# Performance work log

Hardware: AMD Instinct MI355X
Metric: run time of the kernel (lower is better)

The kernel has to match this reference:

```python
import jax, jax.numpy as jnp
import numpy as np

N = 6144
IN_F = 256
OUT_F = 64
ALPHA = 0.2  # leaky relu slope
NEG_INF = -9e15
ADJ_DENSITY = 0.01


def setup_inputs() -> dict:
    key = jax.random.key(0)
    kx, ka, kw, kat, ks, ke = jax.random.split(key, 6)
    x = jax.random.normal(kx, (N, IN_F), dtype=jnp.float32)
    adj = (jax.random.uniform(ka, (N, N)) < ADJ_DENSITY).astype(jnp.float32)
    adj = adj.at[jnp.arange(N), jnp.arange(N)].set(0.0)
    # xavier-uniform-ish init scale (gain 1.414)
    def xavier(k, shape):
        fan_in, fan_out = shape[0], shape[1]
        lim = 1.414 * np.sqrt(6.0 / (fan_in + fan_out))
        return jax.random.uniform(k, shape, minval=-lim, maxval=lim, dtype=jnp.float32)
    W = xavier(kw, (IN_F, OUT_F))
    a = xavier(kat, (2 * OUT_F, 1))
    W_si = xavier(ks, (1, 1))
    W_ei = xavier(ke, (1, 1))
    return {"x": x, "adj": adj, "W": W, "a": a, "W_si": W_si, "W_ei": W_ei}


def reference(x, adj, W, a, W_si, W_ei):
    # h: [N, F_out]
    h = x @ W
    # additive GAT score: e[i,j] = leakyrelu(Wh1[i] + Wh2[j])
    Wh1 = h @ a[:OUT_F, :]           # [N, 1]
    Wh2 = h @ a[OUT_F:, :]           # [N, 1]
    e = jax.nn.leaky_relu(Wh1 + Wh2.T, negative_slope=ALPHA)  # [N, N]
    # adjacency-power topology bias
    adj2 = adj @ adj
    adj3 = adj2 @ adj
    adj_w = adj + adj2 + adj3
    adj_w = adj_w.at[jnp.arange(N), jnp.arange(N)].set(0.0)
    e = jnp.abs(W_ei) * e + jnp.abs(W_si) * adj_w
    # masked softmax over neighbors (row-wise)
    scores = jnp.where(adj > 0, e, NEG_INF)
    attention = jax.nn.softmax(scores, axis=1)
    # dropout omitted (eval mode / training=False)
    h_prime = attention @ h
    return jax.nn.elu(h_prime)
```

## Files before the change

### kernel.cpp

```cpp
#include <hip/hip_runtime.h>
#include <math.h>

#define N 6144
#define MAXD 128
#define NWORDS 96
#define NW32 192

typedef unsigned long long u64;
typedef unsigned int u32;
typedef unsigned char u8;
typedef float f4 __attribute__((ext_vector_type(4)));


__device__ __forceinline__ int a_addr(int j) {
    int vdx = (j & ~255) | ((j & 3) << 6) | ((j >> 2) & 63);
    return (((vdx >> 2) & 7) << 10) | ((vdx >> 5) << 2) | (vdx & 3);
}

#define FA(s, c, a, b, ci) { u32 _t = (a) ^ (b); (s) = _t ^ (ci); (c) = ((a) & (b)) | ((ci) & _t); }

template <int START>
__device__ __forceinline__ void badd_from(u32* p, u32 cy) {
    #pragma unroll
    for (int q = START; q < 6; ++q) { u32 x = p[q] & cy; p[q] ^= cy; cy = x; }
    p[6] ^= cy;
}

__device__ __forceinline__ void csa15(u32* p, const u32* x) {
    u32 s0,c0,s1,c1,s2,c2,s3,c3,s4,c4;
    FA(s0,c0, x[0], x[1], x[2]);
    FA(s1,c1, x[3], x[4], x[5]);
    FA(s2,c2, x[6], x[7], x[8]);
    FA(s3,c3, x[9], x[10], x[11]);
    FA(s4,c4, x[12], x[13], x[14]);
    u32 t0,d0,u0,d1;
    FA(t0,d0, s0, s1, s2);
    FA(u0,d1, s3, s4, t0);
    u32 e0,f0,e1,f1,e2,f2;
    FA(e0,f0, c0, c1, c2);
    FA(e1,f1, c3, c4, d0);
    FA(e2,f2, e0, e1, d1);
    u32 g0,h0;
    FA(g0,h0, f0, f1, f2);
    badd_from<0>(p, u0);
    badd_from<1>(p, e2);
    badd_from<2>(p, g0);
    badd_from<3>(p, h0);
}

__device__ __forceinline__ u64 bit_transpose64(u64 x, int lane) {
    const u64 masks[6] = {0xAAAAAAAAAAAAAAAAull, 0xCCCCCCCCCCCCCCCCull,
                          0xF0F0F0F0F0F0F0F0ull, 0xFF00FF00FF00FF00ull,
                          0xFFFF0000FFFF0000ull, 0xFFFFFFFF00000000ull};
    #pragma unroll
    for (int k = 0; k < 6; ++k) {
        int s = 1 << k;
        u64 m = masks[k];
        u64 y = (u64)__shfl_xor((long long)x, s, 64);
        x = (lane & s) ? ((x & m) | ((y & m) >> s))
                       : ((x & ~m) | ((y & ~m) << s));
    }
    return x;
}

__global__ __launch_bounds__(256) void k_gemm_h(
    const float* __restrict__ x, const float* __restrict__ W,
    const float* __restrict__ a,
    float* __restrict__ h, float* __restrict__ Wh1, float* __restrict__ Wh2)
{
    __shared__ float Wl[256 * 64];
    int t = threadIdx.x;
    #pragma unroll
    for (int c = 0; c < 64; ++c) Wl[c * 256 + t] = W[c * 256 + t];
    __syncthreads();

    int w = t >> 6, lane = t & 63;
    int i0 = blockIdx.x * 32 + w * 8;
    const float* xr = x + (long)i0 * 256;

    float acc[8] = {0.f, 0.f, 0.f, 0.f, 0.f, 0.f, 0.f, 0.f};
    for (int k0 = 0; k0 < 256; k0 += 4) {
        float4 xv[8];
        #pragma unroll
        for (int r = 0; r < 8; ++r)
            xv[r] = *(const float4*)(xr + (long)r * 256 + k0);
        #pragma unroll
        for (int kk = 0; kk < 4; ++kk) {
            float wv = Wl[(k0 + kk) * 64 + lane];
            #pragma unroll
            for (int r = 0; r < 8; ++r) {
                float xs = (kk == 0) ? xv[r].x : (kk == 1) ? xv[r].y
                         : (kk == 2) ? xv[r].z : xv[r].w;
                acc[r] = fmaf(xs, wv, acc[r]);
            }
        }
    }

    #pragma unroll
    for (int r = 0; r < 8; ++r) {
        int i = i0 + r;
        h[(long)i * 64 + lane] = acc[r];
        float s1 = acc[r] * a[lane];
        float s2 = acc[r] * a[64 + lane];
        #pragma unroll
        for (int off = 32; off; off >>= 1) {
            s1 += __shfl_xor(s1, off, 64);
            s2 += __shfl_xor(s2, off, 64);
        }
        if (lane == 0) { Wh1[i] = s1; Wh2[i] = s2; }
    }
}

__global__ __launch_bounds__(256) void k_build(
    const float* __restrict__ adj,
    u64* __restrict__ rowbits, int* __restrict__ row_cnt, int* __restrict__ row_list)
{
    int i = blockIdx.x;
    int t = threadIdx.x, w = t >> 6, lane = t & 63;
    __shared__ int wtot[4];

    const f4* ar = (const f4*)(adj + (long)i * N) + (w * 6) * 64;

    f4 v[6];
    #pragma unroll
    for (int c = 0; c < 6; ++c)
        v[c] = __builtin_nontemporal_load(ar + c * 64 + lane);

    u64 m[6][4];
    #pragma unroll
    for (int c = 0; c < 6; ++c) {
        m[c][0] = __ballot(v[c].x != 0.0f);
        m[c][1] = __ballot(v[c].y != 0.0f);
        m[c][2] = __ballot(v[c].z != 0.0f);
        m[c][3] = __ballot(v[c].w != 0.0f);
    }

    int tot = 0;
    #pragma unroll
    for (int c = 0; c < 6; ++c) {
        #pragma unroll
        for (int p = 0; p < 4; ++p) tot += __popcll(m[c][p]);
    }
    if (lane == 0) wtot[w] = tot;
    __syncthreads();
    int base = 0;
    #pragma unroll
    for (int q = 0; q < 4; ++q) if (q < w) base += wtot[q];

    u64* rb = rowbits + (long)i * NWORDS + w * 24;
    #pragma unroll
    for (int c = 0; c < 6; ++c) {
        #pragma unroll
        for (int p = 0; p < 4; ++p) {
            u64 mm = m[c][p];
            if (lane == 0) rb[c * 4 + p] = mm;
            if ((mm >> lane) & 1ull) {
                int rank = __popcll(mm & ((1ull << lane) - 1ull));
                int s = base + rank;
                int j = (w * 6 + c) * 256 + (lane << 2) + p;
                if (s < MAXD) row_list[(long)i * MAXD + s] = j;
            }
            base += __popcll(mm);
        }
    }
    if (t == 0) {
        int tt = wtot[0] + wtot[1] + wtot[2] + wtot[3];
        row_cnt[i] = tt < 127 ? tt : 127;
    }
}

__global__ __launch_bounds__(256) void k_trans(
    const u64* __restrict__ rowbits, u64* __restrict__ colbits)
{
    int w = threadIdx.x >> 6, lane = threadIdx.x & 63;
    int tile = blockIdx.x * 4 + w;
    int tr = tile / 96, tc = tile - tr * 96;
    u64 x = rowbits[(long)(tr * 64 + lane) * NWORDS + tc];
    x = bit_transpose64(x, lane);
    colbits[(long)(tc * 64 + lane) * NWORDS + tr] = x;
}

__global__ __launch_bounds__(256) void k_collist(
    const u64* __restrict__ colbits,
    int* __restrict__ col_cnt, int* __restrict__ col_list)
{
    int w = threadIdx.x >> 6, lane = threadIdx.x & 63;
    int v = blockIdx.x * 4 + w;
    int j = (v & ~255) | ((v & 63) << 2) | ((v >> 6) & 3);

    u64 w0 = 0, w1 = 0;
    if (lane < 48) {
        const u64* p2 = colbits + (long)v * NWORDS + lane * 2;
        w0 = p2[0]; w1 = p2[1];
    }
    int pc = __popcll(w0) + __popcll(w1);
    int incl = pc;
    #pragma unroll
    for (int off = 1; off < 64; off <<= 1) {
        int y = __shfl_up(incl, off, 64);
        if (lane >= off) incl += y;
    }
    int excl = incl - pc;
    int total = __shfl(incl, 63, 64);
    if (lane == 0) col_cnt[j] = total;

    int* cl = col_list + (long)j * MAXD;
    int s = excl;
    int ibase = lane * 128;
    while (w0) {
        int b = __ffsll((long long)w0) - 1; w0 &= w0 - 1;
        if (s < MAXD) cl[s] = ibase + b;
        ++s;
    }
    ibase += 64;
    while (w1) {
        int b = __ffsll((long long)w1) - 1; w1 &= w1 - 1;
        if (s < MAXD) cl[s] = ibase + b;
        ++s;
    }
}

__global__ __launch_bounds__(256) void k_attn(
    const float* __restrict__ h, const float* __restrict__ Wh1, const float* __restrict__ Wh2,
    const u64* __restrict__ rowbits,
    const int* __restrict__ row_cnt, const int* __restrict__ row_list,
    const int* __restrict__ col_cnt, const int* __restrict__ col_list,
    const float* __restrict__ W_si, const float* __restrict__ W_ei,
    float* __restrict__ out)
{
    __shared__ u32 adj2p[8 * 256];
    __shared__ int nbr[MAXD];
    __shared__ int ccbuf[MAXD];
    __shared__ float lrbuf[MAXD];
    __shared__ float ebuf[MAXD];
    __shared__ float part[256];
    __shared__ float sh_max, sh_sum;

    int i = blockIdx.x;
    int t = threadIdx.x, w = t >> 6, lane = t & 63;
    int deg = row_cnt[i];
    deg = deg < 127 ? deg : 127;

    if (deg == 0) {
        float acc = 0.f;
        for (int r = w; r < N; r += 4) acc += h[(long)r * 64 + lane];
        part[t] = acc;
        __syncthreads();
        if (w == 0) {
            float s = part[lane] + part[64 + lane] + part[128 + lane] + part[192 + lane];
            s *= (1.0f / N);
            out[(long)i * 64 + lane] = s > 0.f ? s : expm1f(s);
        }
        return;
    }

    float aWei = fabsf(W_ei[0]);
    float aWsi = fabsf(W_si[0]);

    if (t < deg) {
        int j = row_list[(long)i * MAXD + t];
        nbr[t] = j;
        int cc = col_cnt[j];
        ccbuf[t] = cc < MAXD ? cc : MAXD;
        float z = Wh1[i] + Wh2[j];
        lrbuf[t] = aWei * (z > 0.f ? z : 0.2f * z);
    }

    if (t < NW32) {
        const u32* rb32 = (const u32*)rowbits;
        const int* rl = row_list + (long)i * MAXD;
        u32 p[7] = {0,0,0,0,0,0,0};

        int m = 0;
        for (; m + 15 <= deg; m += 15) {
            u32 x[15];
            #pragma unroll
            for (int q = 0; q < 15; ++q) {
                int j = rl[m + q];
                x[q] = rb32[(long)j * NW32 + t];
            }
            csa15(p, x);
        }
        if (m < deg) {
            u32 x[15];
            #pragma unroll
            for (int q = 0; q < 15; ++q) {
                int mq = m + q;
                int j = rl[mq < deg ? mq : 0];
                u32 vv = rb32[(long)j * NW32 + t];
                x[q] = (mq < deg) ? vv : 0u;
            }
            csa15(p, x);
        }

        #pragma unroll
        for (int g = 0; g < 8; ++g) {
            u32 acc = 0;
            #pragma unroll
            for (int pl = 0; pl < 7; ++pl) {
                u32 nib = (p[pl] >> (4 * g)) & 0xFu;
                acc += (nib * (0x00204081u << pl)) & (0x01010101u << pl);
            }
            adj2p[g * 256 + t] = acc;
        }
    }
    __syncthreads();

    const u8* adj2b = (const u8*)adj2p;

    {
        int g = t >> 3, sub = t & 7;
        for (int e = g; e < deg; e += 32) {
            int j = nbr[e];
            int cc = ccbuf[e];
            const int* cl = col_list + (long)j * MAXD;
            u32 a3 = 0;
            for (int q = sub; q < cc; q += 8) {
                int k = cl[q];
                a3 += (u32)adj2b[a_addr(k)];
            }
            a3 += __shfl_xor(a3, 1, 64);
            a3 += __shfl_xor(a3, 2, 64);
            a3 += __shfl_xor(a3, 4, 64);
            if (sub == 0) {
                u32 a2 = (u32)adj2b[a_addr(j)];
                ebuf[e] = lrbuf[e] + aWsi * (float)(1u + a2 + a3);
            }
        }
    }
    __syncthreads();

    if (w == 0) {
        float v = -3.4e38f;
        for (int idx = lane; idx < deg; idx += 64) v = fmaxf(v, ebuf[idx]);
        #pragma unroll
        for (int off = 32; off; off >>= 1) v = fmaxf(v, __shfl_xor(v, off, 64));
        if (lane == 0) sh_max = v;
    }
    __syncthreads();
    if (t < deg) ebuf[t] = expf(ebuf[t] - sh_max);
    __syncthreads();
    if (w == 0) {
        float s = 0.f;
        for (int idx = lane; idx < deg; idx += 64) s += ebuf[idx];
        #pragma unroll
        for (int off = 32; off; off >>= 1) s += __shfl_xor(s, off, 64);
        if (lane == 0) sh_sum = s;
    }
    __syncthreads();

    float acc0 = 0.f, acc1 = 0.f;
    int e = w;
    for (; e + 4 < deg; e += 8) {
        acc0 = fmaf(ebuf[e],     h[(long)nbr[e]     * 64 + lane], acc0);
        acc1 = fmaf(ebuf[e + 4], h[(long)nbr[e + 4] * 64 + lane], acc1);
    }
    if (e < deg)
        acc0 = fmaf(ebuf[e], h[(long)nbr[e] * 64 + lane], acc0);
    part[t] = acc0 + acc1;
    __syncthreads();
    if (w == 0) {
        float s = part[lane] + part[64 + lane] + part[128 + lane] + part[192 + lane];
        s /= sh_sum;
        out[(long)i * 64 + lane] = s > 0.f ? s : expm1f(s);
    }
}

extern "C" void kernel_launch(void* const* d_in, const int* in_sizes, int n_in,
                              void* d_out, int out_size, void* d_ws, size_t ws_size,
                              hipStream_t stream) {
    const float* x    = (const float*)d_in[0];
    const float* adj  = (const float*)d_in[1];
    const float* W    = (const float*)d_in[2];
    const float* a    = (const float*)d_in[3];
    const float* W_si = (const float*)d_in[4];
    const float* W_ei = (const float*)d_in[5];
    float* out = (float*)d_out;

    char* ws = (char*)d_ws;
    size_t off = 0;
    auto alloc = [&](size_t bytes) -> void* {
        void* p = ws + off;
        off += (bytes + 255) & ~(size_t)255;
        return p;
    };
    u64*   rowbits  = (u64*)  alloc((size_t)N * NWORDS * sizeof(u64));
    u64*   colbits  = (u64*)  alloc((size_t)N * NWORDS * sizeof(u64));
    float* h        = (float*)alloc((size_t)N * 64 * sizeof(float));
    float* Wh1      = (float*)alloc((size_t)N * sizeof(float));
    float* Wh2      = (float*)alloc((size_t)N * sizeof(float));
    int*   row_cnt  = (int*)  alloc((size_t)N * sizeof(int));
    int*   row_list = (int*)  alloc((size_t)N * MAXD * sizeof(int));
    int*   col_cnt  = (int*)  alloc((size_t)N * sizeof(int));
    int*   col_list = (int*)  alloc((size_t)N * MAXD * sizeof(int));

    k_gemm_h <<<N / 32, 256, 0, stream>>>(x, W, a, h, Wh1, Wh2);
    k_build  <<<N, 256, 0, stream>>>(adj, rowbits, row_cnt, row_list);
    k_trans  <<<(96 * 96) / 4, 256, 0, stream>>>(rowbits, colbits);
    k_collist<<<N / 4, 256, 0, stream>>>(colbits, col_cnt, col_list);
    k_attn   <<<N, 256, 0, stream>>>(h, Wh1, Wh2, rowbits, row_cnt, row_list,
                                     col_cnt, col_list, W_si, W_ei, out);
}
```

Measured before the change: 307.1 us.

## Build column adjacency lists with atomics in k_build, drop transpose kernels

Column neighbor lists are now filled directly in the row-scan kernel: each set bit does an atomicAdd on the column's counter and writes the row index into that column's list. This removes the bit-transpose and column-list kernels, the colbits buffer and two launches, and adds a memset of the counters. Column lists are no longer sorted, so any downstream code that assumes ordering or a deterministic order could see different summation order. Roughly 377K scattered atomics are added.

```diff
diff --git a/kernel.cpp b/kernel.cpp
--- a/kernel.cpp
+++ b/kernel.cpp
@@ -48,21 +48,6 @@
     badd_from<3>(p, h0);
 }
 
-__device__ __forceinline__ u64 bit_transpose64(u64 x, int lane) {
-    const u64 masks[6] = {0xAAAAAAAAAAAAAAAAull, 0xCCCCCCCCCCCCCCCCull,
-                          0xF0F0F0F0F0F0F0F0ull, 0xFF00FF00FF00FF00ull,
-                          0xFFFF0000FFFF0000ull, 0xFFFFFFFF00000000ull};
-    #pragma unroll
-    for (int k = 0; k < 6; ++k) {
-        int s = 1 << k;
-        u64 m = masks[k];
-        u64 y = (u64)__shfl_xor((long long)x, s, 64);
-        x = (lane & s) ? ((x & m) | ((y & m) >> s))
-                       : ((x & ~m) | ((y & ~m) << s));
-    }
-    return x;
-}
-
 __global__ __launch_bounds__(256) void k_gemm_h(
     const float* __restrict__ x, const float* __restrict__ W,
     const float* __restrict__ a,
@@ -113,7 +98,8 @@
 
 __global__ __launch_bounds__(256) void k_build(
     const float* __restrict__ adj,
-    u64* __restrict__ rowbits, int* __restrict__ row_cnt, int* __restrict__ row_list)
+    u64* __restrict__ rowbits, int* __restrict__ row_cnt, int* __restrict__ row_list,
+    int* __restrict__ col_cnt, int* __restrict__ col_list)
 {
     int i = blockIdx.x;
     int t = threadIdx.x, w = t >> 6, lane = t & 63;
@@ -159,6 +145,8 @@
                 int s = base + rank;
                 int j = (w * 6 + c) * 256 + (lane << 2) + p;
                 if (s < MAXD) row_list[(long)i * MAXD + s] = j;
+                int slot = atomicAdd(&col_cnt[j], 1);
+                if (slot < MAXD) col_list[(long)j * MAXD + slot] = i;
             }
             base += __popcll(mm);
         }
@@ -166,57 +154,6 @@
     if (t == 0) {
         int tt = wtot[0] + wtot[1] + wtot[2] + wtot[3];
         row_cnt[i] = tt < 127 ? tt : 127;
-    }
-}
-
-__global__ __launch_bounds__(256) void k_trans(
-    const u64* __restrict__ rowbits, u64* __restrict__ colbits)
-{
-    int w = threadIdx.x >> 6, lane = threadIdx.x & 63;
-    int tile = blockIdx.x * 4 + w;
-    int tr = tile / 96, tc = tile - tr * 96;
-    u64 x = rowbits[(long)(tr * 64 + lane) * NWORDS + tc];
-    x = bit_transpose64(x, lane);
-    colbits[(long)(tc * 64 + lane) * NWORDS + tr] = x;
-}
-
-__global__ __launch_bounds__(256) void k_collist(
-    const u64* __restrict__ colbits,
-    int* __restrict__ col_cnt, int* __restrict__ col_list)
-{
-    int w = threadIdx.x >> 6, lane = threadIdx.x & 63;
-    int v = blockIdx.x * 4 + w;
-    int j = (v & ~255) | ((v & 63) << 2) | ((v >> 6) & 3);
-
-    u64 w0 = 0, w1 = 0;
-    if (lane < 48) {
-        const u64* p2 = colbits + (long)v * NWORDS + lane * 2;
-        w0 = p2[0]; w1 = p2[1];
-    }
-    int pc = __popcll(w0) + __popcll(w1);
-    int incl = pc;
-    #pragma unroll
-    for (int off = 1; off < 64; off <<= 1) {
-        int y = __shfl_up(incl, off, 64);
-        if (lane >= off) incl += y;
-    }
-    int excl = incl - pc;
-    int total = __shfl(incl, 63, 64);
-    if (lane == 0) col_cnt[j] = total;
-
-    int* cl = col_list + (long)j * MAXD;
-    int s = excl;
-    int ibase = lane * 128;
-    while (w0) {
-        int b = __ffsll((long long)w0) - 1; w0 &= w0 - 1;
-        if (s < MAXD) cl[s] = ibase + b;
-        ++s;
-    }
-    ibase += 64;
-    while (w1) {
-        int b = __ffsll((long long)w1) - 1; w1 &= w1 - 1;
-        if (s < MAXD) cl[s] = ibase + b;
-        ++s;
     }
 }
 
@@ -385,7 +322,6 @@
         return p;
     };
     u64*   rowbits  = (u64*)  alloc((size_t)N * NWORDS * sizeof(u64));
-    u64*   colbits  = (u64*)  alloc((size_t)N * NWORDS * sizeof(u64));
     float* h        = (float*)alloc((size_t)N * 64 * sizeof(float));
     float* Wh1      = (float*)alloc((size_t)N * sizeof(float));
     float* Wh2      = (float*)alloc((size_t)N * sizeof(float));
@@ -394,10 +330,10 @@
     int*   col_cnt  = (int*)  alloc((size_t)N * sizeof(int));
     int*   col_list = (int*)  alloc((size_t)N * MAXD * sizeof(int));
 
+    hipMemsetAsync(col_cnt, 0, (size_t)N * sizeof(int), stream);
+
     k_gemm_h <<<N / 32, 256, 0, stream>>>(x, W, a, h, Wh1, Wh2);
-    k_build  <<<N, 256, 0, stream>>>(adj, rowbits, row_cnt, row_list);
-    k_trans  <<<(96 * 96) / 4, 256, 0, stream>>>(rowbits, colbits);
-    k_collist<<<N / 4, 256, 0, stream>>>(colbits, col_cnt, col_list);
+    k_build  <<<N, 256, 0, stream>>>(adj, rowbits, row_cnt, row_list, col_cnt, col_list);
     k_attn   <<<N, 256, 0, stream>>>(h, Wh1, Wh2, rowbits, row_cnt, row_list,
                                      col_cnt, col_list, W_si, W_ei, out);
 }
```

Result: slower. 321.8 us (+4.8%).

## Merge bit-transpose and feature GEMM into one kernel launch

Applied to the files above, without the earlier changes.

The standalone x@W GEMM kernel is removed and its work is appended as extra blocks of the bit-transpose kernel, so one launch covers both and they overlap on the GPU. The GEMM is restructured to 8 rows per block, with x rows staged in shared memory and W loaded in two 128-row halves, giving two accumulators per thread. This saves a launch and fills idle CUs during the small transpose. The trade-off is less register reuse of W per row and more W reloads across the greater number of blocks.

```diff
diff --git a/kernel.cpp b/kernel.cpp
--- a/kernel.cpp
+++ b/kernel.cpp
@@ -63,54 +63,6 @@
     return x;
 }
 
-__global__ __launch_bounds__(256) void k_gemm_h(
-    const float* __restrict__ x, const float* __restrict__ W,
-    const float* __restrict__ a,
-    float* __restrict__ h, float* __restrict__ Wh1, float* __restrict__ Wh2)
-{
-    __shared__ float Wl[256 * 64];
-    int t = threadIdx.x;
-    #pragma unroll
-    for (int c = 0; c < 64; ++c) Wl[c * 256 + t] = W[c * 256 + t];
-    __syncthreads();
-
-    int w = t >> 6, lane = t & 63;
-    int i0 = blockIdx.x * 32 + w * 8;
-    const float* xr = x + (long)i0 * 256;
-
-    float acc[8] = {0.f, 0.f, 0.f, 0.f, 0.f, 0.f, 0.f, 0.f};
-    for (int k0 = 0; k0 < 256; k0 += 4) {
-        float4 xv[8];
-        #pragma unroll
-        for (int r = 0; r < 8; ++r)
-            xv[r] = *(const float4*)(xr + (long)r * 256 + k0);
-        #pragma unroll
-        for (int kk = 0; kk < 4; ++kk) {
-            float wv = Wl[(k0 + kk) * 64 + lane];
-            #pragma unroll
-            for (int r = 0; r < 8; ++r) {
-                float xs = (kk == 0) ? xv[r].x : (kk == 1) ? xv[r].y
-                         : (kk == 2) ? xv[r].z : xv[r].w;
-                acc[r] = fmaf(xs, wv, acc[r]);
-            }
-        }
-    }
-
-    #pragma unroll
-    for (int r = 0; r < 8; ++r) {
-        int i = i0 + r;
-        h[(long)i * 64 + lane] = acc[r];
-        float s1 = acc[r] * a[lane];
-        float s2 = acc[r] * a[64 + lane];
-        #pragma unroll
-        for (int off = 32; off; off >>= 1) {
-            s1 += __shfl_xor(s1, off, 64);
-            s2 += __shfl_xor(s2, off, 64);
-        }
-        if (lane == 0) { Wh1[i] = s1; Wh2[i] = s2; }
-    }
-}
-
 __global__ __launch_bounds__(256) void k_build(
     const float* __restrict__ adj,
     u64* __restrict__ rowbits, int* __restrict__ row_cnt, int* __restrict__ row_list)
@@ -169,15 +121,75 @@
     }
 }
 
-__global__ __launch_bounds__(256) void k_trans(
-    const u64* __restrict__ rowbits, u64* __restrict__ colbits)
+__global__ __launch_bounds__(256) void k_trans_gemm(
+    const u64* __restrict__ rowbits, u64* __restrict__ colbits,
+    const float* __restrict__ x, const float* __restrict__ W,
+    const float* __restrict__ a,
+    float* __restrict__ h, float* __restrict__ Wh1, float* __restrict__ Wh2)
 {
-    int w = threadIdx.x >> 6, lane = threadIdx.x & 63;
-    int tile = blockIdx.x * 4 + w;
-    int tr = tile / 96, tc = tile - tr * 96;
-    u64 x = rowbits[(long)(tr * 64 + lane) * NWORDS + tc];
-    x = bit_transpose64(x, lane);
-    colbits[(long)(tc * 64 + lane) * NWORDS + tr] = x;
+    __shared__ float Wl[128 * 64];
+    __shared__ float xt[8][256];
+
+    int t = threadIdx.x, w = t >> 6, lane = t & 63;
+    int bid = blockIdx.x;
+
+    if (bid < 2304) {
+        int tile = bid * 4 + w;
+        int tr = tile / 96, tc = tile - tr * 96;
+        u64 v = rowbits[(long)(tr * 64 + lane) * NWORDS + tc];
+        v = bit_transpose64(v, lane);
+        colbits[(long)(tc * 64 + lane) * NWORDS + tr] = v;
+        return;
+    }
+
+    long i0 = (long)(bid - 2304) * 8;
+
+    {
+        const float4* xs = (const float4*)(x + i0 * 256);
+        float4* xd = (float4*)&xt[0][0];
+        xd[t]       = xs[t];
+        xd[256 + t] = xs[256 + t];
+    }
+
+    float acc0 = 0.f, acc1 = 0.f;
+    int r0 = w * 2;
+
+    #pragma unroll
+    for (int half = 0; half < 2; ++half) {
+        __syncthreads();
+        {
+            const float4* Ws = (const float4*)(W + half * 128 * 64);
+            float4* Wd = (float4*)Wl;
+            #pragma unroll
+            for (int q = 0; q < 8; ++q) Wd[q * 256 + t] = Ws[q * 256 + t];
+        }
+        __syncthreads();
+        const float* xr0 = &xt[r0][half * 128];
+        const float* xr1 = &xt[r0 + 1][half * 128];
+        #pragma unroll 8
+        for (int kk = 0; kk < 128; ++kk) {
+            float wv = Wl[kk * 64 + lane];
+            acc0 = fmaf(xr0[kk], wv, acc0);
+            acc1 = fmaf(xr1[kk], wv, acc1);
+        }
+    }
+
+    h[(i0 + r0)     * 64 + lane] = acc0;
+    h[(i0 + r0 + 1) * 64 + lane] = acc1;
+    float a1 = a[lane], a2 = a[64 + lane];
+    float s10 = acc0 * a1, s20 = acc0 * a2;
+    float s11 = acc1 * a1, s21 = acc1 * a2;
+    #pragma unroll
+    for (int off = 32; off; off >>= 1) {
+        s10 += __shfl_xor(s10, off, 64);
+        s20 += __shfl_xor(s20, off, 64);
+        s11 += __shfl_xor(s11, off, 64);
+        s21 += __shfl_xor(s21, off, 64);
+    }
+    if (lane == 0) {
+        Wh1[i0 + r0]     = s10;  Wh2[i0 + r0]     = s20;
+        Wh1[i0 + r0 + 1] = s11;  Wh2[i0 + r0 + 1] = s21;
+    }
 }
 
 __global__ __launch_bounds__(256) void k_collist(
@@ -394,10 +406,9 @@
     int*   col_cnt  = (int*)  alloc((size_t)N * sizeof(int));
     int*   col_list = (int*)  alloc((size_t)N * MAXD * sizeof(int));
 
-    k_gemm_h <<<N / 32, 256, 0, stream>>>(x, W, a, h, Wh1, Wh2);
-    k_build  <<<N, 256, 0, stream>>>(adj, rowbits, row_cnt, row_list);
-    k_trans  <<<(96 * 96) / 4, 256, 0, stream>>>(rowbits, colbits);
-    k_collist<<<N / 4, 256, 0, stream>>>(colbits, col_cnt, col_list);
-    k_attn   <<<N, 256, 0, stream>>>(h, Wh1, Wh2, rowbits, row_cnt, row_list,
-                                     col_cnt, col_list, W_si, W_ei, out);
-}
+    k_build     <<<N, 256, 0, stream>>>(adj, rowbits, row_cnt, row_list);
+    k_trans_gemm<<<2304 + 768, 256, 0, stream>>>(rowbits, colbits, x, W, a, h, Wh1, Wh2);
+    k_collist   <<<N / 4, 256, 0, stream>>>(colbits, col_cnt, col_list);
+    k_attn      <<<N, 256, 0, stream>>>(h, Wh1, Wh2, rowbits, row_cnt, row_list,
+                                        col_cnt, col_list, W_si, W_ei, out);
+}
```

New measurement: 298.2 us. 1.03x faster.
